# Kernel tuning notes

Hardware: AMD Instinct MI355X
Metric: run time of the kernel (lower is better)

The kernel has to match this reference:

```python
import jax, jax.numpy as jnp
import numpy as np

FILTER_SIZE = 27           # filter_size (K + 2)
K = FILTER_SIZE - 2        # sampled neighbors per central node
FEAT = 512                 # feature_dim
HID = 512                  # hidden_dim
NUM_NODES = 100000         # node-id universe for the features() embedding
B = 20000                  # batch of central nodes
ALPHA = 0.2                # leaky relu slope


def _star_eigvec(fs):
    # eigenvectors of I - D A D for the star graph on `fs` nodes (node 0 = hub)
    A = np.zeros((fs, fs))
    A[0, 1:] = 1.0
    A[1:, 0] = 1.0
    D = np.eye(fs)
    D[0, 0] = (fs - 1) ** (-0.5)
    L = np.eye(fs) - D @ A @ D
    _, u = np.linalg.eigh(L)
    return u.astype(np.float32)


def setup_inputs() -> dict:
    key = jax.random.key(0)
    k1, k2, k3, k4, k5 = jax.random.split(key, 5)
    nodes = jax.random.randint(k1, (B,), 0, NUM_NODES)
    neigh = jax.random.randint(k2, (B, K), 0, NUM_NODES)
    feat_table = jax.random.normal(k3, (NUM_NODES, FEAT), dtype=jnp.float32)
    # xavier_uniform for W [FEAT, HID] and a [2*HID]
    limW = float(np.sqrt(6.0 / (FEAT + HID)))
    W = jax.random.uniform(k4, (FEAT, HID), minval=-limW, maxval=limW, dtype=jnp.float32)
    lima = float(np.sqrt(6.0 / (1 + 2 * HID)))
    a_vec = jax.random.uniform(k5, (2 * HID,), minval=-lima, maxval=lima, dtype=jnp.float32)
    U = jnp.asarray(_star_eigvec(FILTER_SIZE))
    return {"nodes": nodes, "neigh": neigh, "feat_table": feat_table,
            "W": W, "a_vec": a_vec, "U": U}


def reference(nodes, neigh, feat_table, W, a_vec, U):
    # project features: input2 (central), input1 (neighbors)
    h_ct = feat_table[nodes] @ W                              # [B, H]
    h_nb = jnp.einsum('bkf,fh->bkh', feat_table[neigh], W)    # [B, K, H]
    # GAT-style edge scores: a @ [h_ct ; h_nb]
    s_ct = h_ct @ a_vec[:HID]                                 # [B]
    s_nb = h_nb @ a_vec[HID:]                                 # [B, K]
    logits = s_ct[:, None] + s_nb                             # [B, K]
    lrelu = jnp.where(logits > 0, logits, ALPHA * logits)
    edge_e = jnp.exp(-lrelu)                                  # [B, K]
    # per-row normalization (equals dense a1 rowsum: neighbors per row distinct)
    attn = edge_e / jnp.sum(edge_e, axis=1, keepdims=True)    # [B, K]
    # mask1: slots 1..K of each filter_size block hold attn * h_nb
    mask = attn[..., None] * h_nb                             # [B, K, H]
    m = jnp.pad(mask, ((0, 0), (1, 1), (0, 0)))               # [B, FILTER_SIZE, H]
    mt = jnp.swapaxes(m, 1, 2)                                # [B, H, FILTER_SIZE]
    # spectral transform: (mt @ U @ U^T) @ ones[FILTER_SIZE,1]
    avg = jnp.ones((FILTER_SIZE, 1), dtype=m.dtype)
    temp = ((mt @ U) @ U.T) @ avg                             # [B, H, 1]
    out = jnp.squeeze(temp, axis=-1)                          # [B, H]
    return jax.nn.relu(out)
```

## Files before the change

kernel.cpp:

```cpp
#include <hip/hip_runtime.h>
#include <stdint.h>
#include <string.h>

#define FEAT 512
#define HID 512
#define KNB 25
#define FS 27
#define ALPHA 0.2f

typedef short bf16x8 __attribute__((ext_vector_type(8)));
typedef float f32x4 __attribute__((ext_vector_type(4)));

__device__ __forceinline__ float bf2f(unsigned short u) {
    union { unsigned int i; float f; } x; x.i = ((unsigned int)u) << 16; return x.f;
}
__device__ __forceinline__ unsigned short f2bf(float f) {
    unsigned int x = __float_as_uint(f);
    unsigned int r = (x + 0x7fffu + ((x >> 16) & 1u)) >> 16;
    return (unsigned short)r;
}
__device__ __forceinline__ float ldf(const void* base, size_t idx, bool isf32) {
    return isf32 ? ((const float*)base)[idx] : bf2f(((const unsigned short*)base)[idx]);
}

__global__ void detect_dtype(const void* __restrict__ feat, int* __restrict__ flag) {
    __shared__ int cnt;
    if (threadIdx.x == 0) cnt = 0;
    __syncthreads();
    const unsigned short* u = (const unsigned short*)feat;
    int c = 0;
    for (int i = threadIdx.x; i < 2048; i += 256) {
        float av = fabsf(bf2f(u[i]));
        if (!(av < 1e4f)) c++;
    }
    atomicAdd(&cnt, c);
    __syncthreads();
    if (threadIdx.x == 0) *flag = (cnt > 16) ? 1 : 0;
}

__global__ void prep_pq(const void* __restrict__ W, const void* __restrict__ a_vec,
                        const int* __restrict__ flag,
                        float* __restrict__ p, float* __restrict__ q) {
    bool isf32 = (*flag != 0);
    int f = blockIdx.x;
    int lane = threadIdx.x;
    float accp = 0.f, accq = 0.f;
    #pragma unroll
    for (int j = 0; j < 8; ++j) {
        int h = lane * 8 + j;
        float wv = ldf(W, (size_t)f * HID + h, isf32);
        accq += wv * ldf(a_vec, h, isf32);
        accp += wv * ldf(a_vec, HID + h, isf32);
    }
    #pragma unroll
    for (int off = 32; off > 0; off >>= 1) {
        accp += __shfl_down(accp, off);
        accq += __shfl_down(accq, off);
    }
    if (lane == 0) { p[f] = accp; q[f] = accq; }
}

__global__ void prep_M(const void* __restrict__ U, const int* __restrict__ flag,
                       float* __restrict__ Mv) {
    __shared__ float cs[FS];
    bool isf32 = (*flag != 0);
    int t = threadIdx.x;
    if (t < FS) {
        float c = 0.f;
        for (int i = 0; i < FS; ++i) c += ldf(U, i * FS + t, isf32);
        cs[t] = c;
    }
    __syncthreads();
    if (t < FS) {
        float m = 0.f;
        for (int j = 0; j < FS; ++j) m += ldf(U, t * FS + j, isf32) * cs[j];
        Mv[t] = m;
    }
}

__global__ void transposeW(const void* __restrict__ W, const int* __restrict__ flag,
                           unsigned short* __restrict__ Wt) {
    bool isf32 = (*flag != 0);
    int idx = blockIdx.x * blockDim.x + threadIdx.x;
    int n = idx >> 9, k = idx & (HID - 1);
    Wt[idx] = f2bf(ldf(W, (size_t)k * HID + n, isf32));
}

__global__ __launch_bounds__(256) void attn_gather(
    const void* __restrict__ feat, const int* __restrict__ nodes,
    const int* __restrict__ neigh, const float* __restrict__ p,
    const float* __restrict__ q, const float* __restrict__ Mv,
    const int* __restrict__ flag, unsigned short* __restrict__ g) {
    __shared__ __attribute__((aligned(16))) unsigned short ldsF[KNB * FEAT];
    __shared__ float ldsS[KNB + 1];
    bool isf32 = (*flag != 0);
    int b = blockIdx.x;
    int t = threadIdx.x;
    int wave = t >> 6, lane = t & 63;
    for (int r = wave; r < KNB + 1; r += 4) {
        int id = (r == 0) ? nodes[b] : neigh[(size_t)b * KNB + (r - 1)];
        float vals[8];
        if (isf32) {
            const float4* row = (const float4*)((const float*)feat + (size_t)id * FEAT) + lane * 2;
            float4 v0 = row[0], v1 = row[1];
            vals[0] = v0.x; vals[1] = v0.y; vals[2] = v0.z; vals[3] = v0.w;
            vals[4] = v1.x; vals[5] = v1.y; vals[6] = v1.z; vals[7] = v1.w;
        } else {
            uint4 v = *((const uint4*)((const unsigned short*)feat + (size_t)id * FEAT) + lane);
            unsigned int w4[4] = {v.x, v.y, v.z, v.w};
            #pragma unroll
            for (int j = 0; j < 4; ++j) {
                vals[2 * j]     = bf2f((unsigned short)(w4[j] & 0xffffu));
                vals[2 * j + 1] = bf2f((unsigned short)(w4[j] >> 16));
            }
        }
        if (r > 0) {
            unsigned short o[8];
            #pragma unroll
            for (int j = 0; j < 8; ++j) o[j] = f2bf(vals[j]);
            *(uint4*)(&ldsF[(r - 1) * FEAT + lane * 8]) = *(const uint4*)o;
        }
        const float* vec = ((r == 0) ? q : p) + lane * 8;
        float acc = 0.f;
        #pragma unroll
        for (int j = 0; j < 8; ++j) acc += vals[j] * vec[j];
        #pragma unroll
        for (int off = 32; off > 0; off >>= 1) acc += __shfl_down(acc, off);
        if (lane == 0) ldsS[r] = acc;
    }
    __syncthreads();
    float s0 = ldsS[0];
    float w[KNB];
    float Z = 0.f;
    #pragma unroll
    for (int k = 0; k < KNB; ++k) {
        float l = s0 + ldsS[k + 1];
        float lr = l > 0.f ? l : ALPHA * l;
        float e = __expf(-lr);
        w[k] = e;
        Z += e;
    }
    float inv = 1.f / Z;
    #pragma unroll
    for (int k = 0; k < KNB; ++k) w[k] *= inv * Mv[k + 1];
    float acc0 = 0.f, acc1 = 0.f;
    #pragma unroll
    for (int k = 0; k < KNB; ++k) {
        unsigned int v = *(const unsigned int*)(&ldsF[k * FEAT + 2 * t]);
        acc0 += w[k] * bf2f((unsigned short)(v & 0xffffu));
        acc1 += w[k] * bf2f((unsigned short)(v >> 16));
    }
    unsigned int o = ((unsigned int)f2bf(acc1) << 16) | (unsigned int)f2bf(acc0);
    *(unsigned int*)(&g[(size_t)b * FEAT + 2 * t]) = o;
}

__global__ __launch_bounds__(256) void gemm_relu(
    const unsigned short* __restrict__ G, const unsigned short* __restrict__ Wt,
    const int* __restrict__ flag, void* __restrict__ out, int M) {
    __shared__ __attribute__((aligned(16))) unsigned short As[64 * 72];
    __shared__ __attribute__((aligned(16))) unsigned short Bs[64 * 72];
    bool isf32 = (*flag != 0);
    int t = threadIdx.x;
    int mBase = blockIdx.y * 64;
    int nBase = blockIdx.x * 64;
    int wave = t >> 6, lane = t & 63;
    int mOff = (wave & 1) * 32, nOff = (wave >> 1) * 32;
    f32x4 acc00 = {0.f, 0.f, 0.f, 0.f}, acc01 = {0.f, 0.f, 0.f, 0.f};
    f32x4 acc10 = {0.f, 0.f, 0.f, 0.f}, acc11 = {0.f, 0.f, 0.f, 0.f};
    int lr = t >> 2;
    int seg = (t & 3) * 16;
    int fr = lane & 15, quad = lane >> 4;
    for (int k0 = 0; k0 < FEAT; k0 += 64) {
        uint4 av0 = {0u, 0u, 0u, 0u}, av1 = {0u, 0u, 0u, 0u};
        int gr = mBase + lr;
        if (gr < M) {
            const unsigned short* s = G + (size_t)gr * FEAT + k0 + seg;
            av0 = *(const uint4*)s;
            av1 = *(const uint4*)(s + 8);
        }
        *(uint4*)(&As[lr * 72 + seg]) = av0;
        *(uint4*)(&As[lr * 72 + seg + 8]) = av1;
        const unsigned short* bs = Wt + (size_t)(nBase + lr) * FEAT + k0 + seg;
        *(uint4*)(&Bs[lr * 72 + seg]) = *(const uint4*)bs;
        *(uint4*)(&Bs[lr * 72 + seg + 8]) = *(const uint4*)(bs + 8);
        __syncthreads();
        #pragma unroll
        for (int kk = 0; kk < 64; kk += 32) {
            bf16x8 a0 = *(const bf16x8*)(&As[(mOff + fr) * 72 + kk + quad * 8]);
            bf16x8 a1 = *(const bf16x8*)(&As[(mOff + 16 + fr) * 72 + kk + quad * 8]);
            bf16x8 b0 = *(const bf16x8*)(&Bs[(nOff + fr) * 72 + kk + quad * 8]);
            bf16x8 b1 = *(const bf16x8*)(&Bs[(nOff + 16 + fr) * 72 + kk + quad * 8]);
            acc00 = __builtin_amdgcn_mfma_f32_16x16x32_bf16(a0, b0, acc00, 0, 0, 0);
            acc01 = __builtin_amdgcn_mfma_f32_16x16x32_bf16(a0, b1, acc01, 0, 0, 0);
            acc10 = __builtin_amdgcn_mfma_f32_16x16x32_bf16(a1, b0, acc10, 0, 0, 0);
            acc11 = __builtin_amdgcn_mfma_f32_16x16x32_bf16(a1, b1, acc11, 0, 0, 0);
        }
        __syncthreads();
    }
    int col = lane & 15, qr = (lane >> 4) * 4;
    #pragma unroll
    for (int sel = 0; sel < 4; ++sel) {
        f32x4 a = (sel == 0) ? acc00 : (sel == 1) ? acc01 : (sel == 2) ? acc10 : acc11;
        int mt = sel >> 1, nt = sel & 1;
        #pragma unroll
        for (int i = 0; i < 4; ++i) {
            int row = mBase + mOff + mt * 16 + qr + i;
            if (row < M) {
                int cn = nBase + nOff + nt * 16 + col;
                float v = a[i];
                v = v > 0.f ? v : 0.f;
                size_t off = (size_t)row * HID + cn;
                if (isf32) ((float*)out)[off] = v;
                else ((unsigned short*)out)[off] = f2bf(v);
            }
        }
    }
}

extern "C" void kernel_launch(void* const* d_in, const int* in_sizes, int n_in,
                              void* d_out, int out_size, void* d_ws, size_t ws_size,
                              hipStream_t stream) {
    const int* nodes = (const int*)d_in[0];
    const int* neigh = (const int*)d_in[1];
    const void* feat = d_in[2];
    const void* W = d_in[3];
    const void* a_vec = d_in[4];
    const void* U = d_in[5];
    int B = in_sizes[0];

    char* ws = (char*)d_ws;
    int* flag = (int*)ws;
    float* p = (float*)(ws + 256);
    float* q = (float*)(ws + 256 + 2048);
    float* Mv = (float*)(ws + 256 + 4096);
    unsigned short* Wt = (unsigned short*)(ws + 4608);
    unsigned short* g = (unsigned short*)(ws + 4608 + FEAT * HID * 2);

    detect_dtype<<<1, 256, 0, stream>>>(feat, flag);
    prep_pq<<<FEAT, 64, 0, stream>>>(W, a_vec, flag, p, q);
    prep_M<<<1, 32, 0, stream>>>(U, flag, Mv);
    transposeW<<<(FEAT * HID) / 256, 256, 0, stream>>>(W, flag, Wt);
    attn_gather<<<B, 256, 0, stream>>>(feat, nodes, neigh, p, q, Mv, flag, g);
    dim3 gg(HID / 64, (B + 63) / 64);
    gemm_relu<<<gg, 256, 0, stream>>>(g, Wt, flag, d_out, B);
}
```

Measured before the change: 460.9 us.

## Precompute per-node scores and bf16 table, gather with one wave per row

Adds a pass over the whole 100k-row feature table that converts it to bf16 and computes both attention score dot products (p and q) for every node once. A new gather kernel then uses one wave per batch row: it looks up the precomputed scores, does the softmax with wave shuffles, and accumulates the weighted neighbor rows straight from global memory without staging them in LDS. This removes the repeated per-edge score dot products and the LDS staging, and halves the gather traffic when the input is fp32. In exchange it touches the whole table (about 200MB read for fp32) even though only about 520k rows are gathered. It also needs a large workspace, and falls back to the old kernel when the workspace is too small.

```diff
diff --git a/kernel.cpp b/kernel.cpp
--- a/kernel.cpp
+++ b/kernel.cpp
@@ -6,6 +6,7 @@
 #define HID 512
 #define KNB 25
 #define FS 27
+#define NNODES 100000
 #define ALPHA 0.2f
 
 typedef short bf16x8 __attribute__((ext_vector_type(8)));
@@ -84,6 +85,89 @@
     int idx = blockIdx.x * blockDim.x + threadIdx.x;
     int n = idx >> 9, k = idx & (HID - 1);
     Wt[idx] = f2bf(ldf(W, (size_t)k * HID + n, isf32));
+}
+
+__global__ __launch_bounds__(256) void convert_score(
+    const void* __restrict__ feat, const float* __restrict__ p,
+    const float* __restrict__ q, const int* __restrict__ flag,
+    unsigned short* __restrict__ featbf, float* __restrict__ sp,
+    float* __restrict__ sq, int nRows) {
+    bool isf32 = (*flag != 0);
+    int wave = threadIdx.x >> 6, lane = threadIdx.x & 63;
+    int row = blockIdx.x * 4 + wave;
+    if (row >= nRows) return;
+    float vals[8];
+    if (isf32) {
+        const float4* src = (const float4*)((const float*)feat + (size_t)row * FEAT) + lane * 2;
+        float4 v0 = src[0], v1 = src[1];
+        vals[0] = v0.x; vals[1] = v0.y; vals[2] = v0.z; vals[3] = v0.w;
+        vals[4] = v1.x; vals[5] = v1.y; vals[6] = v1.z; vals[7] = v1.w;
+        unsigned short o[8];
+        #pragma unroll
+        for (int j = 0; j < 8; ++j) o[j] = f2bf(vals[j]);
+        *(uint4*)(&featbf[(size_t)row * FEAT + lane * 8]) = *(const uint4*)o;
+    } else {
+        uint4 v = *((const uint4*)((const unsigned short*)feat + (size_t)row * FEAT) + lane);
+        unsigned int w4[4] = {v.x, v.y, v.z, v.w};
+        #pragma unroll
+        for (int j = 0; j < 4; ++j) {
+            vals[2 * j]     = __uint_as_float(w4[j] << 16);
+            vals[2 * j + 1] = __uint_as_float(w4[j] & 0xffff0000u);
+        }
+    }
+    float accp = 0.f, accq = 0.f;
+    const float* pv = p + lane * 8;
+    const float* qv = q + lane * 8;
+    #pragma unroll
+    for (int j = 0; j < 8; ++j) { accp += vals[j] * pv[j]; accq += vals[j] * qv[j]; }
+    #pragma unroll
+    for (int off = 32; off > 0; off >>= 1) {
+        accp += __shfl_down(accp, off);
+        accq += __shfl_down(accq, off);
+    }
+    if (lane == 0) { sp[row] = accp; sq[row] = accq; }
+}
+
+__global__ __launch_bounds__(256) void attn_gather2(
+    const void* __restrict__ feat, const unsigned short* __restrict__ featbf,
+    const int* __restrict__ nodes, const int* __restrict__ neigh,
+    const float* __restrict__ sp, const float* __restrict__ sq,
+    const float* __restrict__ Mv, const int* __restrict__ flag,
+    unsigned short* __restrict__ g, int B) {
+    bool isf32 = (*flag != 0);
+    const unsigned short* F = isf32 ? featbf : (const unsigned short*)feat;
+    int wave = threadIdx.x >> 6, lane = threadIdx.x & 63;
+    int b = blockIdx.x * 4 + wave;
+    if (b >= B) return;
+    int id = 0; float e = 0.f;
+    if (lane < KNB) {
+        id = neigh[(size_t)b * KNB + lane];
+        float l = sq[nodes[b]] + sp[id];
+        float lr = l > 0.f ? l : ALPHA * l;
+        e = __expf(-lr);
+    }
+    float Z = e;
+    #pragma unroll
+    for (int off = 16; off > 0; off >>= 1) Z += __shfl_down(Z, off);
+    Z = __shfl(Z, 0);
+    float w = (lane < KNB) ? e * (1.f / Z) * Mv[lane + 1] : 0.f;
+    float acc[8] = {0.f, 0.f, 0.f, 0.f, 0.f, 0.f, 0.f, 0.f};
+    #pragma unroll
+    for (int k = 0; k < KNB; ++k) {
+        int idk = __builtin_amdgcn_readlane(id, k);
+        float wk = __uint_as_float((unsigned int)__builtin_amdgcn_readlane(__float_as_int(w), k));
+        uint4 v = *((const uint4*)(F + (size_t)idk * FEAT) + lane);
+        unsigned int w4[4] = {v.x, v.y, v.z, v.w};
+        #pragma unroll
+        for (int j = 0; j < 4; ++j) {
+            acc[2 * j]     += wk * __uint_as_float(w4[j] << 16);
+            acc[2 * j + 1] += wk * __uint_as_float(w4[j] & 0xffff0000u);
+        }
+    }
+    unsigned short o[8];
+    #pragma unroll
+    for (int j = 0; j < 8; ++j) o[j] = f2bf(acc[j]);
+    *(uint4*)(&g[(size_t)b * FEAT + lane * 8]) = *(const uint4*)o;
 }
 
 __global__ __launch_bounds__(256) void attn_gather(
@@ -234,13 +318,23 @@
     float* q = (float*)(ws + 256 + 2048);
     float* Mv = (float*)(ws + 256 + 4096);
     unsigned short* Wt = (unsigned short*)(ws + 4608);
-    unsigned short* g = (unsigned short*)(ws + 4608 + FEAT * HID * 2);
+    unsigned short* g = (unsigned short*)(ws + 4608 + (size_t)FEAT * HID * 2);
+    size_t gEnd = 4608 + (size_t)FEAT * HID * 2 + (size_t)B * FEAT * 2;
+    float* sp = (float*)(ws + gEnd);
+    float* sq = (float*)(ws + gEnd + (size_t)NNODES * 4);
+    unsigned short* featbf = (unsigned short*)(ws + gEnd + (size_t)NNODES * 8);
+    size_t need = gEnd + (size_t)NNODES * 8 + (size_t)NNODES * FEAT * 2;
 
     detect_dtype<<<1, 256, 0, stream>>>(feat, flag);
     prep_pq<<<FEAT, 64, 0, stream>>>(W, a_vec, flag, p, q);
     prep_M<<<1, 32, 0, stream>>>(U, flag, Mv);
     transposeW<<<(FEAT * HID) / 256, 256, 0, stream>>>(W, flag, Wt);
-    attn_gather<<<B, 256, 0, stream>>>(feat, nodes, neigh, p, q, Mv, flag, g);
+    if (ws_size >= need) {
+        convert_score<<<(NNODES + 3) / 4, 256, 0, stream>>>(feat, p, q, flag, featbf, sp, sq, NNODES);
+        attn_gather2<<<(B + 3) / 4, 256, 0, stream>>>(feat, featbf, nodes, neigh, sp, sq, Mv, flag, g, B);
+    } else {
+        attn_gather<<<B, 256, 0, stream>>>(feat, nodes, neigh, p, q, Mv, flag, g);
+    }
     dim3 gg(HID / 64, (B + 63) / 64);
     gemm_relu<<<gg, 256, 0, stream>>>(g, Wt, flag, d_out, B);
 }
```

After: 426.1 us. -7.6%, faster.
